# Performance work log

Hardware: AMD Instinct MI355X
Metric: run time of the kernel (lower is better)

The kernel has to match this reference:

```python
import jax, jax.numpy as jnp
import numpy as np

BATCH_SIZE = 4096
NUM_CAMS = 64
D_FEAT = 512
EPS = 1e-16  # standard safe-sqrt epsilon used by utils.euclidean_distance_matrix


def setup_inputs() -> dict:
    key = jax.random.key(0)
    x = jax.random.normal(key, (BATCH_SIZE, D_FEAT), dtype=jnp.float32)
    # calc_idx: row i indexes the (frprcam-1) same-camera off-diagonal slots,
    # all rows in a block share idx = arange(frprcam-1) + block_start
    frprcam = BATCH_SIZE // NUM_CAMS
    uf = frprcam - 1
    block_start = (np.arange(BATCH_SIZE) // frprcam) * frprcam
    idxs = jnp.asarray(block_start[:, None] + np.arange(uf)[None, :], dtype=jnp.int32)
    return {"x": x, "idxs": idxs}


def _euclidean_distance_matrix(x):
    # ||xi - xj||: gram trick with zero-masking so sqrt is safe at 0
    dot = x @ x.T                                  # [B,B]
    sq = jnp.diagonal(dot)                         # [B]
    d2 = jax.nn.relu(sq[:, None] - 2.0 * dot + sq[None, :])
    zero = (d2 == 0.0).astype(x.dtype)
    return jnp.sqrt(d2 + zero * EPS) * (1.0 - zero)


def reference(x, idxs):
    bs = x.shape[0]
    dist = _euclidean_distance_matrix(x)           # [B,B]
    # drop the diagonal: flatten()[1:].view(B-1, B+1)[:, :-1] trick
    offdiag = dist.reshape(-1)[1:].reshape(bs - 1, bs + 1)[:, :-1].reshape(bs, bs - 1)
    logits = jax.nn.softmax(-offdiag, axis=1)      # [B,B-1]
    p = jnp.take_along_axis(logits, idxs, axis=1).sum(axis=1)  # [B]
    return (-jnp.log(p)).sum() / bs
```

## Files before the change

kernel.cpp:

```cpp
#include <hip/hip_runtime.h>
#include <hip/hip_bf16.h>

#define BATCH 4096
#define DFEAT 512
#define TM 128
#define TN 128
#define BK 64
#define NB (BATCH / TM)
#define NPAIR (NB * (NB + 1) / 2)

typedef __attribute__((ext_vector_type(8))) __bf16 bf16x8;
typedef __attribute__((ext_vector_type(4))) float f32x4;

__device__ inline ushort f2bf(float f) {
    uint u = __float_as_uint(f);
    uint r = (u + 0x7FFFu + ((u >> 16) & 1u)) >> 16;
    return (ushort)r;
}

__global__ __launch_bounds__(256) void prep_kernel(
        const float* __restrict__ x, ushort* __restrict__ xb,
        float* __restrict__ sqx, float* __restrict__ num, float* __restrict__ den,
        float* __restrict__ out) {
    int t = blockIdx.x * 256 + threadIdx.x;
    if (t < BATCH) { num[t] = 0.0f; den[t] = 0.0f; }
    if (t == 0) out[0] = 0.0f;
    int wid = threadIdx.x >> 6, lane = threadIdx.x & 63;
    int row = blockIdx.x * 4 + wid;
    const float* xr = x + (size_t)row * DFEAT + lane * 8;
    float4 v0 = *(const float4*)(xr);
    float4 v1 = *(const float4*)(xr + 4);
    float f[8] = {v0.x, v0.y, v0.z, v0.w, v1.x, v1.y, v1.z, v1.w};
    float s = 0.0f;
#pragma unroll
    for (int i = 0; i < 8; i++) s += f[i] * f[i];
    uint us[4];
#pragma unroll
    for (int i = 0; i < 4; i++)
        us[i] = (uint)f2bf(f[2 * i]) | ((uint)f2bf(f[2 * i + 1]) << 16);
    *(uint4*)&xb[(size_t)row * DFEAT + lane * 8] = *(uint4*)us;
#pragma unroll
    for (int m = 32; m; m >>= 1) s += __shfl_xor(s, m, 64);
    if (lane == 0) sqx[row] = s;
}

__global__ __launch_bounds__(256) void dist_kernel(
        const ushort* __restrict__ xb, const float* __restrict__ sqx,
        float* __restrict__ num, float* __restrict__ den) {
    __shared__ __align__(16) ushort As[TM * BK];
    __shared__ __align__(16) ushort Bs[TN * BK];

    int idx = blockIdx.x;
    float nb5 = (float)NB + 0.5f;
    int rb = (int)(nb5 - sqrtf(nb5 * nb5 - 2.0f * (float)idx));
    while (rb > 0 && rb * NB - rb * (rb - 1) / 2 > idx) rb--;
    while ((rb + 1) * NB - (rb + 1) * rb / 2 <= idx) rb++;
    int cb = rb + idx - (rb * NB - rb * (rb - 1) / 2);

    const int rowbase = rb * TM, colbase = cb * TN;
    const int tid = threadIdx.x;
    const int wid = tid >> 6, lane = tid & 63;
    const int wr = wid >> 1, wc = wid & 1;
    const int l15 = lane & 15, l4 = lane >> 4;

    f32x4 acc[4][4] = {};

    for (int kb = 0; kb < DFEAT; kb += BK) {
#pragma unroll
        for (int q = 0; q < 4; q++) {
            int u = q * 256 + tid;
            int r = u >> 3, c = (u & 7) * 8;
            const ushort* ga = &xb[(size_t)(rowbase + r) * DFEAT + kb + c];
            const ushort* gb = &xb[(size_t)(colbase + r) * DFEAT + kb + c];
            ushort* la = &As[(q * 256 + wid * 64) * 8];
            ushort* lb = &Bs[(q * 256 + wid * 64) * 8];
            __builtin_amdgcn_global_load_lds(
                (const __attribute__((address_space(1))) void*)ga,
                (__attribute__((address_space(3))) void*)la, 16, 0, 0);
            __builtin_amdgcn_global_load_lds(
                (const __attribute__((address_space(1))) void*)gb,
                (__attribute__((address_space(3))) void*)lb, 16, 0, 0);
        }
        __syncthreads();
#pragma unroll
        for (int kk = 0; kk < BK; kk += 32) {
            bf16x8 a[4], b[4];
#pragma unroll
            for (int mi = 0; mi < 4; mi++)
                a[mi] = *(const bf16x8*)&As[(wr * 64 + mi * 16 + l15) * BK + kk + l4 * 8];
#pragma unroll
            for (int ni = 0; ni < 4; ni++)
                b[ni] = *(const bf16x8*)&Bs[(wc * 64 + ni * 16 + l15) * BK + kk + l4 * 8];
#pragma unroll
            for (int mi = 0; mi < 4; mi++)
#pragma unroll
                for (int ni = 0; ni < 4; ni++)
                    acc[mi][ni] = __builtin_amdgcn_mfma_f32_16x16x32_bf16(
                        a[mi], b[ni], acc[mi][ni], 0, 0, 0);
        }
        __syncthreads();
    }

    float sj[4];
#pragma unroll
    for (int ni = 0; ni < 4; ni++) sj[ni] = sqx[colbase + wc * 64 + ni * 16 + l15];

    if (rb == cb) {
#pragma unroll
        for (int mi = 0; mi < 4; mi++) {
#pragma unroll
            for (int r = 0; r < 4; r++) {
                const int i = rowbase + wr * 64 + mi * 16 + 4 * l4 + r;
                const float si = sqx[i];
                float np = 0.0f, dp = 0.0f;
#pragma unroll
                for (int ni = 0; ni < 4; ni++) {
                    const int j = colbase + wc * 64 + ni * 16 + l15;
                    float d2 = fmaxf(si + sj[ni] - 2.0f * acc[mi][ni][r], 0.0f);
                    float e = (i == j) ? 0.0f : __expf(-sqrtf(d2));
                    dp += e;
                    np += ((i >> 6) == (j >> 6)) ? e : 0.0f;
                }
#pragma unroll
                for (int m = 1; m <= 8; m <<= 1) {
                    np += __shfl_xor(np, m, 64);
                    dp += __shfl_xor(dp, m, 64);
                }
                if (l15 == 0) {
                    atomicAdd(&num[i], np);
                    atomicAdd(&den[i], dp);
                }
            }
        }
    } else {
        float cde[4] = {0.0f, 0.0f, 0.0f, 0.0f};
#pragma unroll
        for (int mi = 0; mi < 4; mi++) {
#pragma unroll
            for (int r = 0; r < 4; r++) {
                const int i = rowbase + wr * 64 + mi * 16 + 4 * l4 + r;
                const float si = sqx[i];
                float dp = 0.0f;
#pragma unroll
                for (int ni = 0; ni < 4; ni++) {
                    float d2 = fmaxf(si + sj[ni] - 2.0f * acc[mi][ni][r], 0.0f);
                    float e = __expf(-sqrtf(d2));
                    dp += e;
                    cde[ni] += e;
                }
#pragma unroll
                for (int m = 1; m <= 8; m <<= 1) dp += __shfl_xor(dp, m, 64);
                if (l15 == 0) atomicAdd(&den[i], dp);
            }
        }
#pragma unroll
        for (int ni = 0; ni < 4; ni++) {
            float c = cde[ni];
            c += __shfl_xor(c, 16, 64);
            c += __shfl_xor(c, 32, 64);
            if (l4 == 0) atomicAdd(&den[colbase + wc * 64 + ni * 16 + l15], c);
        }
    }
}

__global__ __launch_bounds__(256) void loss_kernel(
        const float* __restrict__ num, const float* __restrict__ den,
        float* __restrict__ out) {
    __shared__ float red[4];
    int t = blockIdx.x * 256 + threadIdx.x;
    float s = logf(den[t]) - logf(num[t]);
#pragma unroll
    for (int m = 32; m; m >>= 1) s += __shfl_xor(s, m, 64);
    int wid = threadIdx.x >> 6, lane = threadIdx.x & 63;
    if (lane == 0) red[wid] = s;
    __syncthreads();
    if (threadIdx.x == 0)
        atomicAdd(out, (red[0] + red[1] + red[2] + red[3]) * (1.0f / (float)BATCH));
}

extern "C" void kernel_launch(void* const* d_in, const int* in_sizes, int n_in,
                              void* d_out, int out_size, void* d_ws, size_t ws_size,
                              hipStream_t stream) {
    const float* x = (const float*)d_in[0];
    char* ws = (char*)d_ws;
    ushort* xb = (ushort*)ws;
    float* sqx = (float*)(ws + (size_t)BATCH * DFEAT * 2);
    float* num = sqx + BATCH;
    float* den = num + BATCH;
    float* out = (float*)d_out;

    prep_kernel<<<BATCH / 4, 256, 0, stream>>>(x, xb, sqx, num, den, out);
    dist_kernel<<<NPAIR, 256, 0, stream>>>(xb, sqx, num, den);
    loss_kernel<<<BATCH / 256, 256, 0, stream>>>(num, den, out);
}
```

Measured before the change: 104.9 us.

## Double-buffer LDS tiles, XOR-swizzle LDS layout, and remap blocks across XCDs

Splits the K loop into stage and compute phases over two LDS buffers, so the next tile's global-to-LDS loads are issued while the current tile runs through MFMA. The LDS column chunks are XOR-swizzled by row to reduce bank conflicts on the bf16x8 fragment reads. Block indices are also remapped so consecutive tile pairs go to the same XCD, which should improve L2 reuse. The cost is doubled LDS use (64KB), which may lower occupancy. The remap also assumes NPAIR divides evenly by 8 (528/8=66, which holds).

```diff
diff --git a/kernel.cpp b/kernel.cpp
--- a/kernel.cpp
+++ b/kernel.cpp
@@ -8,6 +8,8 @@
 #define BK 64
 #define NB (BATCH / TM)
 #define NPAIR (NB * (NB + 1) / 2)
+#define NXCD 8
+#define CPX (NPAIR / NXCD)
 
 typedef __attribute__((ext_vector_type(8))) __bf16 bf16x8;
 typedef __attribute__((ext_vector_type(4))) float f32x4;
@@ -47,10 +49,12 @@
 __global__ __launch_bounds__(256) void dist_kernel(
         const ushort* __restrict__ xb, const float* __restrict__ sqx,
         float* __restrict__ num, float* __restrict__ den) {
-    __shared__ __align__(16) ushort As[TM * BK];
-    __shared__ __align__(16) ushort Bs[TN * BK];
-
-    int idx = blockIdx.x;
+    __shared__ __align__(16) ushort As[2][TM * BK];
+    __shared__ __align__(16) ushort Bs[2][TN * BK];
+
+    int bid = blockIdx.x;
+    int idx = (bid % NXCD) * CPX + bid / NXCD;
+
     float nb5 = (float)NB + 0.5f;
     int rb = (int)(nb5 - sqrtf(nb5 * nb5 - 2.0f * (float)idx));
     while (rb > 0 && rb * NB - rb * (rb - 1) / 2 > idx) rb--;
@@ -65,15 +69,16 @@
 
     f32x4 acc[4][4] = {};
 
-    for (int kb = 0; kb < DFEAT; kb += BK) {
+    auto stage = [&](int buf, int kb) {
 #pragma unroll
         for (int q = 0; q < 4; q++) {
             int u = q * 256 + tid;
-            int r = u >> 3, c = (u & 7) * 8;
-            const ushort* ga = &xb[(size_t)(rowbase + r) * DFEAT + kb + c];
-            const ushort* gb = &xb[(size_t)(colbase + r) * DFEAT + kb + c];
-            ushort* la = &As[(q * 256 + wid * 64) * 8];
-            ushort* lb = &Bs[(q * 256 + wid * 64) * 8];
+            int r = u >> 3;
+            int cch = ((u & 7) ^ (r & 7)) << 3;
+            const ushort* ga = &xb[(size_t)(rowbase + r) * DFEAT + kb + cch];
+            const ushort* gb = &xb[(size_t)(colbase + r) * DFEAT + kb + cch];
+            ushort* la = &As[buf][(q * 256 + wid * 64) * 8];
+            ushort* lb = &Bs[buf][(q * 256 + wid * 64) * 8];
             __builtin_amdgcn_global_load_lds(
                 (const __attribute__((address_space(1))) void*)ga,
                 (__attribute__((address_space(3))) void*)la, 16, 0, 0);
@@ -81,16 +86,24 @@
                 (const __attribute__((address_space(1))) void*)gb,
                 (__attribute__((address_space(3))) void*)lb, 16, 0, 0);
         }
-        __syncthreads();
+    };
+
+    auto compute = [&](int buf) {
 #pragma unroll
         for (int kk = 0; kk < BK; kk += 32) {
             bf16x8 a[4], b[4];
 #pragma unroll
-            for (int mi = 0; mi < 4; mi++)
-                a[mi] = *(const bf16x8*)&As[(wr * 64 + mi * 16 + l15) * BK + kk + l4 * 8];
-#pragma unroll
-            for (int ni = 0; ni < 4; ni++)
-                b[ni] = *(const bf16x8*)&Bs[(wc * 64 + ni * 16 + l15) * BK + kk + l4 * 8];
+            for (int mi = 0; mi < 4; mi++) {
+                int ra = wr * 64 + mi * 16 + l15;
+                a[mi] = *(const bf16x8*)
+                    &As[buf][ra * BK + ((((kk >> 3) + l4) ^ (ra & 7)) << 3)];
+            }
+#pragma unroll
+            for (int ni = 0; ni < 4; ni++) {
+                int rc = wc * 64 + ni * 16 + l15;
+                b[ni] = *(const bf16x8*)
+                    &Bs[buf][rc * BK + ((((kk >> 3) + l4) ^ (rc & 7)) << 3)];
+            }
 #pragma unroll
             for (int mi = 0; mi < 4; mi++)
 #pragma unroll
@@ -98,8 +111,19 @@
                     acc[mi][ni] = __builtin_amdgcn_mfma_f32_16x16x32_bf16(
                         a[mi], b[ni], acc[mi][ni], 0, 0, 0);
         }
+    };
+
+    stage(0, 0);
+    __syncthreads();
+    int cur = 0;
+#pragma unroll 1
+    for (int t = 0; t < DFEAT / BK - 1; t++) {
+        stage(cur ^ 1, (t + 1) * BK);
+        compute(cur);
         __syncthreads();
+        cur ^= 1;
     }
+    compute(cur);
 
     float sj[4];
 #pragma unroll
```

Measured after the change: 102.7 us. 1.02x faster.
